# Kernel optimization log

Hardware: AMD Instinct MI355X
Metric: run time of the kernel (lower is better)

Reference implementation:

```python
import jax, jax.numpy as jnp
import numpy as np

B, C, E, H = 1024, 1024, 128, 8
INF = 1.0e8


def setup_inputs() -> dict:
    key = jax.random.key(0)
    ks = jax.random.split(key, 16)
    f32 = jnp.float32
    inp = {
        "h": jax.random.normal(ks[0], (B, C, E), dtype=f32),
        "h_N": jax.random.normal(ks[1], (B, 1, E), dtype=f32),
        "h_prev": jax.random.normal(ks[2], (B, 1, E), dtype=f32),
        "h_0": jax.random.normal(ks[3], (B, 1, E), dtype=f32),
        "mask": jax.random.randint(ks[4], (B, C), 0, 2, dtype=jnp.int32),
        # Linear weights stored (out, in) like torch; y = x @ W.T + b
        "Qw": jax.random.normal(ks[5], (E, 3 * E), dtype=f32) * 0.05,
        "Qb": jnp.zeros((E,), dtype=f32),
        "Vw": jax.random.normal(ks[6], (E, E), dtype=f32) * 0.05,
        "Vb": jnp.zeros((E,), dtype=f32),
        "Wow": jax.random.normal(ks[7], (E, E), dtype=f32) * 0.05,
        "Wob": jnp.zeros((E,), dtype=f32),
        "Qfw": jax.random.normal(ks[8], (E, E), dtype=f32) * 0.05,
        "Qfb": jnp.zeros((E,), dtype=f32),
        "Kfw": jax.random.normal(ks[9], (E, E), dtype=f32) * 0.05,
        "Kfb": jnp.zeros((E,), dtype=f32),
    }
    return inp


def reference(h, h_N, h_prev, h_0, mask, Qw, Qb, Vw, Vb, Wow, Wob, Qfw, Qfb, Kfw, Kfb):
    batch, city, embed = h.shape
    heads = H
    eh = embed // heads  # head_dim = 16
    maskf = mask.astype(h.dtype)

    h_c = jnp.concatenate((h_N, h_prev, h_0), axis=2)        # (B,1,3E)
    q = h_c @ Qw.T + Qb                                      # (B,1,E)
    v = h @ Vw.T + Vb                                        # (B,C,E)
    # NOTE: source uses v for keys too (k_h = reshape(v, ...)); K(h) is dead code.
    q_h = q.reshape(batch, 1, heads, eh).transpose(0, 2, 1, 3)   # (B,H,1,eh)
    v_h = v.reshape(batch, city, heads, eh).transpose(0, 2, 1, 3)  # (B,H,C,eh)

    dot = jnp.einsum("bhqe,bhce->bhqc", q_h, v_h) / jnp.sqrt(jnp.asarray(eh, h.dtype))
    dot = dot - maskf[:, None, None, :] * INF                # additive mask
    att = jax.nn.softmax(dot, axis=-1)                       # (B,H,1,C)
    context = jnp.einsum("bhqc,bhce->bhqe", att, v_h)        # (B,H,1,eh)
    context = context.transpose(0, 2, 1, 3).reshape(batch, 1, embed)

    dec_out = context @ Wow.T + Wob                          # (B,1,E)
    qf = dec_out @ Qfw.T + Qfb                               # (B,1,E)
    kf = h @ Kfw.T + Kfb                                     # (B,C,E)
    logits = jnp.einsum("bqe,bce->bc", qf, kf) / jnp.sqrt(jnp.asarray(embed, h.dtype))
    logits = 10.0 * jnp.tanh(logits) - maskf * INF           # (B,C)
    return logits
```

## Files before the change

kernel.cpp:

```cpp
#include <hip/hip_runtime.h>
#include <hip/hip_bf16.h>

#define NB 1024
#define NC 1024
#define NE 128
#define NH 8
#define EH 16
#define INFV 1.0e8f
#define TILE 64
#define LSTRIDE 132

__device__ __forceinline__ float wredmax64(float v) {
#pragma unroll
    for (int m = 32; m >= 1; m >>= 1) v = fmaxf(v, __shfl_xor(v, m, 64));
    return v;
}
__device__ __forceinline__ float wredsum64(float v) {
#pragma unroll
    for (int m = 32; m >= 1; m >>= 1) v += __shfl_xor(v, m, 64);
    return v;
}

__global__ __launch_bounds__(512, 4)
void decoder_mha_fused(const float* __restrict__ h, const float* __restrict__ hN,
                       const float* __restrict__ hprev, const float* __restrict__ h0,
                       const int* __restrict__ mask,
                       const float* __restrict__ Qw, const float* __restrict__ Qb,
                       const float* __restrict__ Vw, const float* __restrict__ Vb,
                       const float* __restrict__ Wow, const float* __restrict__ Wob,
                       const float* __restrict__ Qfw, const float* __restrict__ Qfb,
                       const float* __restrict__ Kfw, const float* __restrict__ Kfb,
                       float* __restrict__ out) {
    __shared__ __align__(16) float hs[TILE * LSTRIDE];
    __shared__ __align__(16) float wdot[NH * NE];
    __shared__ __align__(16) float hc[3 * NE];
    __shared__ __align__(16) float qv[NE];
    __shared__ __align__(16) float hbarn[NH * NE];
    __shared__ __align__(16) float ctx[NE];
    __shared__ __align__(16) float dec[NE];
    __shared__ __align__(16) float qfv[NE];
    __shared__ __align__(16) float qk[NE];
    __shared__ __align__(16) float red[NE];
    __shared__ float d0q[NH];
    __shared__ float qb0s;

    const int b = blockIdx.x;
    const int tid = threadIdx.x;
    const int lane = tid & 63;
    const int wid = tid >> 6;
    const int hl = lane & 31;
    const int hi = lane >> 5;

    const float* hb = h + (size_t)b * NC * NE;

    if (tid < 128)      hc[tid] = hN[b * NE + tid];
    else if (tid < 256) hc[tid] = hprev[b * NE + (tid - 128)];
    else if (tid < 384) hc[tid] = h0[b * NE + (tid - 256)];
    __syncthreads();

    if (tid < NE) {
        float acc = Qb[tid];
        const float* qr = Qw + tid * 384;
#pragma unroll 4
        for (int k = 0; k < 384; k += 4) {
            float4 w4 = *(const float4*)(qr + k);
            float4 x4 = *(const float4*)(hc + k);
            acc += w4.x * x4.x + w4.y * x4.y + w4.z * x4.z + w4.w * x4.w;
        }
        qv[tid] = acc;
    }
    __syncthreads();

    for (int idx = tid; idx < NH * NE; idx += 512) {
        int hh = idx >> 7, d = idx & 127;
        float acc = 0.f;
#pragma unroll
        for (int e = 0; e < EH; ++e)
            acc += qv[hh * EH + e] * Vw[(hh * EH + e) * NE + d];
        wdot[idx] = acc;
    }
    if (tid < NH) {
        float acc = 0.f;
#pragma unroll
        for (int e = 0; e < EH; ++e) acc += qv[tid * EH + e] * Vb[tid * EH + e];
        d0q[tid] = acc * 0.25f;
    }
    __syncthreads();

    float m = -3.0e38f, l = 0.f;
    float hb0 = 0.f, hb1 = 0.f, hb2 = 0.f, hb3 = 0.f;

    float4 r0 = *(const float4*)(hb + tid * 4);
    float4 r1 = *(const float4*)(hb + 2048 + tid * 4);
    float4 r2 = *(const float4*)(hb + 4096 + tid * 4);
    float4 r3 = *(const float4*)(hb + 6144 + tid * 4);

    const int c0 = tid >> 5;
    const int dd = (tid & 31) * 4;

    for (int t = 0; t < NC / TILE; ++t) {
        __syncthreads();
        *(float4*)(hs + (c0)      * LSTRIDE + dd) = r0;
        *(float4*)(hs + (c0 + 16) * LSTRIDE + dd) = r1;
        *(float4*)(hs + (c0 + 32) * LSTRIDE + dd) = r2;
        *(float4*)(hs + (c0 + 48) * LSTRIDE + dd) = r3;
        __syncthreads();

        if (t < NC / TILE - 1) {
            const float* src = hb + (t + 1) * TILE * NE;
            r0 = *(const float4*)(src + tid * 4);
            r1 = *(const float4*)(src + 2048 + tid * 4);
            r2 = *(const float4*)(src + 4096 + tid * 4);
            r3 = *(const float4*)(src + 6144 + tid * 4);
        }

        float acc = 0.f;
        const float* wrow = wdot + wid * NE;
        const float* hrow = hs + lane * LSTRIDE;
#pragma unroll 8
        for (int dq = 0; dq < NE; dq += 4) {
            float4 w4 = *(const float4*)(wrow + dq);
            float4 x4 = *(const float4*)(hrow + dq);
            acc += w4.x * x4.x + w4.y * x4.y + w4.z * x4.z + w4.w * x4.w;
        }
        int mk = mask[b * NC + t * TILE + lane];
        float dt = fmaf(acc, 0.25f, d0q[wid]) - (float)mk * INFV;

        float tmax = wredmax64(dt);
        float mnew = fmaxf(m, tmax);
        float p = __expf(dt - mnew);
        float ts = wredsum64(p);
        float scale = __expf(m - mnew);
        l = l * scale + ts;
        if (mnew > m) { hb0 *= scale; hb1 *= scale; hb2 *= scale; hb3 *= scale; }
        m = mnew;

        const float* hbase = hs + hi * LSTRIDE + hl * 4;
#pragma unroll
        for (int cc = 0; cc < 32; ++cc) {
            float4 x4 = *(const float4*)(hbase + 2 * cc * LSTRIDE);
            float p0 = __uint_as_float(__builtin_amdgcn_readlane(__float_as_uint(p), 2 * cc));
            float p1 = __uint_as_float(__builtin_amdgcn_readlane(__float_as_uint(p), 2 * cc + 1));
            float pv = hi ? p1 : p0;
            hb0 = fmaf(x4.x, pv, hb0);
            hb1 = fmaf(x4.y, pv, hb1);
            hb2 = fmaf(x4.z, pv, hb2);
            hb3 = fmaf(x4.w, pv, hb3);
        }
    }
    hb0 += __shfl_xor(hb0, 32, 64);
    hb1 += __shfl_xor(hb1, 32, 64);
    hb2 += __shfl_xor(hb2, 32, 64);
    hb3 += __shfl_xor(hb3, 32, 64);
    float rl = 1.0f / l;
    if (lane < 32)
        *(float4*)(hbarn + wid * NE + hl * 4) = make_float4(hb0 * rl, hb1 * rl, hb2 * rl, hb3 * rl);
    __syncthreads();

    if (tid < NE) {
        int hh = tid >> 4;
        float acc = Vb[tid];
        const float* vr = Vw + tid * NE;
        const float* hr = hbarn + hh * NE;
#pragma unroll 4
        for (int d = 0; d < NE; d += 4) {
            float4 w4 = *(const float4*)(vr + d);
            float4 x4 = *(const float4*)(hr + d);
            acc += w4.x * x4.x + w4.y * x4.y + w4.z * x4.z + w4.w * x4.w;
        }
        ctx[tid] = acc;
    }
    __syncthreads();
    if (tid < NE) {
        float acc = Wob[tid];
        const float* wr = Wow + tid * NE;
#pragma unroll 4
        for (int d = 0; d < NE; d += 4) {
            float4 w4 = *(const float4*)(wr + d);
            float4 x4 = *(const float4*)(ctx + d);
            acc += w4.x * x4.x + w4.y * x4.y + w4.z * x4.z + w4.w * x4.w;
        }
        dec[tid] = acc;
    }
    __syncthreads();
    if (tid < NE) {
        float acc = Qfb[tid];
        const float* wr = Qfw + tid * NE;
#pragma unroll 4
        for (int d = 0; d < NE; d += 4) {
            float4 w4 = *(const float4*)(wr + d);
            float4 x4 = *(const float4*)(dec + d);
            acc += w4.x * x4.x + w4.y * x4.y + w4.z * x4.z + w4.w * x4.w;
        }
        qfv[tid] = acc;
    }
    __syncthreads();
    if (tid < NE) {
        float acc = 0.f;
#pragma unroll 4
        for (int i = 0; i < NE; ++i) acc += qfv[i] * Kfw[i * NE + tid];
        qk[tid] = acc;
        red[tid] = qfv[tid] * Kfb[tid];
    }
    __syncthreads();
    if (tid == 0) {
        float s = 0.f;
        for (int i = 0; i < NE; ++i) s += red[i];
        qb0s = s;
    }
    __syncthreads();

    const float invsq = 0.0883883476483184f;
    float4 qk4 = *(const float4*)(qk + hl * 4);
    float qb0 = qb0s;
    for (int it = 0; it < 64; ++it) {
        int cpair = wid * 128 + it * 2;
        float4 x4 = *(const float4*)(hb + cpair * NE + lane * 4);
        float pd = qk4.x * x4.x + qk4.y * x4.y + qk4.z * x4.z + qk4.w * x4.w;
#pragma unroll
        for (int mm = 16; mm >= 1; mm >>= 1) pd += __shfl_xor(pd, mm, 64);
        if (hl == 0) {
            int c = cpair + hi;
            float x = (pd + qb0) * invsq;
            float e2 = __expf(2.f * x);
            float th = 1.f - 2.f / (e2 + 1.f);
            float mk = (float)mask[b * NC + c];
            out[(size_t)b * NC + c] = 10.f * th - mk * INFV;
        }
    }
}

extern "C" void kernel_launch(void* const* d_in, const int* in_sizes, int n_in,
                              void* d_out, int out_size, void* d_ws, size_t ws_size,
                              hipStream_t stream) {
    const float* h     = (const float*)d_in[0];
    const float* hN    = (const float*)d_in[1];
    const float* hprev = (const float*)d_in[2];
    const float* h0    = (const float*)d_in[3];
    const int*   mask  = (const int*)d_in[4];
    const float* Qw    = (const float*)d_in[5];
    const float* Qb    = (const float*)d_in[6];
    const float* Vw    = (const float*)d_in[7];
    const float* Vb    = (const float*)d_in[8];
    const float* Wow   = (const float*)d_in[9];
    const float* Wob   = (const float*)d_in[10];
    const float* Qfw   = (const float*)d_in[11];
    const float* Qfb   = (const float*)d_in[12];
    const float* Kfw   = (const float*)d_in[13];
    const float* Kfb   = (const float*)d_in[14];

    decoder_mha_fused<<<dim3(NB), dim3(512), 0, stream>>>(
        h, hN, hprev, h0, mask, Qw, Qb, Vw, Vb, Wow, Wob, Qfw, Qfb, Kfw, Kfb,
        (float*)d_out);
}
```

Measured before the change: 920.8 us.

## Alias scratch buffers onto tile LDS and prefetch mask with next tile

Moves the small per-block scratch arrays (hc, qv, hbarn, ctx, dec, qfv, qk, red, qb0s) into the hs tile buffer, using them only when the tile is not live and adding a barrier before reuse. This shrinks shared memory per block. The launch bound is raised to 8 blocks per CU so more blocks can be resident at once. The mask load for the next tile is also issued together with the h prefetch, which hides its latency. The higher occupancy target may push register use down and cause spills.

```diff
diff --git a/kernel.cpp b/kernel.cpp
--- a/kernel.cpp
+++ b/kernel.cpp
@@ -21,7 +21,7 @@
     return v;
 }
 
-__global__ __launch_bounds__(512, 4)
+__global__ __launch_bounds__(512, 8)
 void decoder_mha_fused(const float* __restrict__ h, const float* __restrict__ hN,
                        const float* __restrict__ hprev, const float* __restrict__ h0,
                        const int* __restrict__ mask,
@@ -33,16 +33,7 @@
                        float* __restrict__ out) {
     __shared__ __align__(16) float hs[TILE * LSTRIDE];
     __shared__ __align__(16) float wdot[NH * NE];
-    __shared__ __align__(16) float hc[3 * NE];
-    __shared__ __align__(16) float qv[NE];
-    __shared__ __align__(16) float hbarn[NH * NE];
-    __shared__ __align__(16) float ctx[NE];
-    __shared__ __align__(16) float dec[NE];
-    __shared__ __align__(16) float qfv[NE];
-    __shared__ __align__(16) float qk[NE];
-    __shared__ __align__(16) float red[NE];
     __shared__ float d0q[NH];
-    __shared__ float qb0s;
 
     const int b = blockIdx.x;
     const int tid = threadIdx.x;
@@ -53,6 +44,8 @@
 
     const float* hb = h + (size_t)b * NC * NE;
 
+    float* hc = hs;
+    float* qv = hs + 384;
     if (tid < 128)      hc[tid] = hN[b * NE + tid];
     else if (tid < 256) hc[tid] = hprev[b * NE + (tid - 128)];
     else if (tid < 384) hc[tid] = h0[b * NE + (tid - 256)];
@@ -94,6 +87,7 @@
     float4 r1 = *(const float4*)(hb + 2048 + tid * 4);
     float4 r2 = *(const float4*)(hb + 4096 + tid * 4);
     float4 r3 = *(const float4*)(hb + 6144 + tid * 4);
+    int mk = mask[b * NC + lane];
 
     const int c0 = tid >> 5;
     const int dd = (tid & 31) * 4;
@@ -106,12 +100,14 @@
         *(float4*)(hs + (c0 + 48) * LSTRIDE + dd) = r3;
         __syncthreads();
 
+        int mk_cur = mk;
         if (t < NC / TILE - 1) {
             const float* src = hb + (t + 1) * TILE * NE;
             r0 = *(const float4*)(src + tid * 4);
             r1 = *(const float4*)(src + 2048 + tid * 4);
             r2 = *(const float4*)(src + 4096 + tid * 4);
             r3 = *(const float4*)(src + 6144 + tid * 4);
+            mk = mask[b * NC + (t + 1) * TILE + lane];
         }
 
         float acc = 0.f;
@@ -123,8 +119,7 @@
             float4 x4 = *(const float4*)(hrow + dq);
             acc += w4.x * x4.x + w4.y * x4.y + w4.z * x4.z + w4.w * x4.w;
         }
-        int mk = mask[b * NC + t * TILE + lane];
-        float dt = fmaf(acc, 0.25f, d0q[wid]) - (float)mk * INFV;
+        float dt = fmaf(acc, 0.25f, d0q[wid]) - (float)mk_cur * INFV;
 
         float tmax = wredmax64(dt);
         float mnew = fmaxf(m, tmax);
@@ -153,6 +148,14 @@
     hb2 += __shfl_xor(hb2, 32, 64);
     hb3 += __shfl_xor(hb3, 32, 64);
     float rl = 1.0f / l;
+    __syncthreads();
+    float* hbarn = hs;
+    float* ctx   = hs + 1024;
+    float* dec   = hs + 1152;
+    float* qfv   = hs + 1280;
+    float* qk    = hs + 1408;
+    float* red   = hs + 1536;
+    float* qb0s  = hs + 1664;
     if (lane < 32)
         *(float4*)(hbarn + wid * NE + hl * 4) = make_float4(hb0 * rl, hb1 * rl, hb2 * rl, hb3 * rl);
     __syncthreads();
@@ -206,13 +209,13 @@
     if (tid == 0) {
         float s = 0.f;
         for (int i = 0; i < NE; ++i) s += red[i];
-        qb0s = s;
+        qb0s[0] = s;
     }
     __syncthreads();
 
     const float invsq = 0.0883883476483184f;
     float4 qk4 = *(const float4*)(qk + hl * 4);
-    float qb0 = qb0s;
+    float qb0 = qb0s[0];
     for (int it = 0; it < 64; ++it) {
         int cpair = wid * 128 + it * 2;
         float4 x4 = *(const float4*)(hb + cpair * NE + lane * 4);
@@ -224,8 +227,8 @@
             float x = (pd + qb0) * invsq;
             float e2 = __expf(2.f * x);
             float th = 1.f - 2.f / (e2 + 1.f);
-            float mk = (float)mask[b * NC + c];
-            out[(size_t)b * NC + c] = 10.f * th - mk * INFV;
+            float mkv = (float)mask[b * NC + c];
+            out[(size_t)b * NC + c] = 10.f * th - mkv * INFV;
         }
     }
 }
```

After: 1.016 ms. +10.3%, slower.
